# Optimization experiments

Hardware: AMD Instinct MI355X
Metric: run time of the kernel (lower is better)

## Reference

```python
import jax, jax.numpy as jnp
from jax import lax
import numpy as np

# init_kwargs (FlowNet-C canonical config)
K = 1      # kernel_size
MD = 20    # max_displacement
S1 = 1     # stride_1 (input stride)
S2 = 2     # stride_2 (displacement stride)
PAD = 20   # spatial zero padding


def setup_inputs() -> dict:
    key = jax.random.key(0)
    k1, k2 = jax.random.split(key)
    shape = (16, 48, 64, 256)  # [B, H, W, C], channels_last
    return {
        "input_a": jax.random.normal(k1, shape, dtype=jnp.float32),
        "input_b": jax.random.normal(k2, shape, dtype=jnp.float32),
    }


def _corr(a, b):
    # FlowNet correlation cost volume (TFA addons_correlation_cost semantics).
    B, H, W, C = a.shape
    rad = MD // S2                      # displacement radius in stride_2 steps
    D = 2 * rad + 1                     # displacements per axis
    rk = (K - 1) // 2                   # kernel radius
    bd = MD + rk                        # border
    oH = H + 2 * (PAD - bd) // S1       # matches layer's compute_output_shape
    oW = W + 2 * (PAD - bd) // S1
    rows = (oH - 1) * S1 + K            # extent of input needed (pre-pool)
    cols = (oW - 1) * S1 + K

    pa = jnp.pad(a, ((0, 0), (PAD, PAD), (PAD, PAD), (0, 0)))
    pb = jnp.pad(b, ((0, 0), (PAD, PAD), (PAD, PAD), (0, 0)))
    # static region of A covering all kernel windows (centers at h*S1+bd)
    a_reg = lax.slice(pa, (0, bd - rk, bd - rk, 0),
                      (B, bd - rk + rows, bd - rk + cols, C))

    def body(_, d):
        # top_channel d -> (tj, ti) row-major, tj vertical as in TFA kernel
        dy = (d // D) * S2 - MD
        dx = (d % D) * S2 - MD
        b_reg = lax.dynamic_slice(pb, (0, bd - rk + dy, bd - rk + dx, 0),
                                  (B, rows, cols, C))
        p = jnp.sum(a_reg * b_reg, axis=-1)           # [B, rows, cols]
        o = lax.reduce_window(p, 0.0, lax.add,
                              (1, K, K), (1, S1, S1), 'VALID')  # [B, oH, oW]
        return None, o

    # remat keeps scan residuals small (slices recomputed in any backward pass)
    _, outs = lax.scan(jax.checkpoint(body), None, jnp.arange(D * D))
    # [D*D, B, oH, oW] -> [B, oH, oW, D*D]; TFA kernel divides by K*K*C
    return jnp.transpose(outs, (1, 2, 3, 0)) / (K * K * C)


def reference(input_a, input_b):
    return _corr(input_a, input_b)
```

## Files before the change

### kernel.cpp

```cpp
#include <hip/hip_runtime.h>
#include <hip/hip_bf16.h>

#define HH    48
#define WW    64
#define CC    256
#define ND    21
#define OUTD  441
#define PITCH 264
#define SROWS 32

typedef __bf16 v8bf16 __attribute__((ext_vector_type(8)));
typedef float  v4f    __attribute__((ext_vector_type(4)));

__global__ __launch_bounds__(384)
void corr_mfma_kernel(const float* __restrict__ A, const float* __restrict__ B,
                      float* __restrict__ out) {
    __shared__ __bf16 Blds[2][SROWS * PITCH];

    const int blk  = blockIdx.x;
    const int b    = blk >> 5;
    const int rem  = blk & 31;
    const int p    = rem & 1;
    const int hpar = (rem >> 1) & 1;
    const int trip = rem >> 2;
    const int h0   = 6 * trip + hpar;

    const int tid  = threadIdx.x;
    const int lane = tid & 63;
    const int wave = tid >> 6;
    const int mt   = wave & 1;
    const int hr   = wave >> 1;
    const int n    = lane & 15;
    const int quad = lane >> 4;

    const int h = h0 + 2 * hr;

    const int i_lo = (h0 >= 21) ? 0 : ((21 - h0) >> 1);
    const int i_hi = min(22, (67 - h0) >> 1);

    for (int r = 0; r < 3; ++r) {
        int hrow  = h0 + 2 * r;
        int tv_lo = max(0, i_lo - r);
        int tv_hi = min(20, i_hi - r);
        float* outr = out + (size_t)(b * HH + hrow) * WW * OUTD;
        for (int tj = 0; tj < ND; ++tj) {
            if (tj >= tv_lo && tj <= tv_hi) continue;
            for (int idx = tid; idx < 32 * ND; idx += 384) {
                int wp = idx / ND, ti = idx - wp * ND;
                int w  = (wp << 1) + p;
                outr[(size_t)w * OUTD + tj * ND + ti] = 0.f;
            }
        }
    }

    v8bf16 afrag[8];
    {
        int w_a = ((mt * 16 + n) << 1) + p;
        const float* arow = A + ((size_t)(b * HH + h) * WW + w_a) * CC;
        #pragma unroll
        for (int kc = 0; kc < 8; ++kc) {
            int c0 = kc * 32 + quad * 8;
            float4 f0 = *(const float4*)(arow + c0);
            float4 f1 = *(const float4*)(arow + c0 + 4);
            v8bf16 af;
            af[0] = (__bf16)f0.x; af[1] = (__bf16)f0.y; af[2] = (__bf16)f0.z; af[3] = (__bf16)f0.w;
            af[4] = (__bf16)f1.x; af[5] = (__bf16)f1.y; af[6] = (__bf16)f1.z; af[7] = (__bf16)f1.w;
            afrag[kc] = af;
        }
    }

    const float* bimg = B + (size_t)(b * HH) * WW * CC + p * CC;
    float4 pf[6];
    auto load_pf = [&](int hb) {
        const float* brow = bimg + (size_t)hb * WW * CC;
        #pragma unroll
        for (int it = 0; it < 6; ++it) {
            int idx = it * 384 + tid;
            if (idx < 2048)
                pf[it] = *(const float4*)(brow + (idx >> 6) * 2 * CC + ((idx & 63) << 2));
        }
    };
    auto store_lds = [&](int buf) {
        #pragma unroll
        for (int it = 0; it < 6; ++it) {
            int idx = it * 384 + tid;
            if (idx < 2048) {
                __bf16* dst = &Blds[buf][(idx >> 6) * PITCH + ((idx & 63) << 2)];
                dst[0] = (__bf16)pf[it].x; dst[1] = (__bf16)pf[it].y;
                dst[2] = (__bf16)pf[it].z; dst[3] = (__bf16)pf[it].w;
            }
        }
    };

    load_pf(h0 - 20 + 2 * i_lo);
    store_lds(0);
    int cur = 0;

    float* outr = out + (size_t)(b * HH + h) * WW * OUTD;

    for (int i = i_lo; i <= i_hi; ++i) {
        if (i < i_hi) load_pf(h0 - 20 + 2 * (i + 1));
        __syncthreads();

        const int tj = i - hr;
        if ((unsigned)tj <= 20u) {
            const __bf16* bbase = &Blds[cur][n * PITCH + quad * 8];
            v4f acc0 = {0.f, 0.f, 0.f, 0.f};
            v4f acc1 = acc0;
            #pragma unroll
            for (int kc = 0; kc < 8; ++kc) {
                v8bf16 bf0 = *(const v8bf16*)(bbase + kc * 32);
                v8bf16 bf1 = *(const v8bf16*)(bbase + 16 * PITCH + kc * 32);
                acc0 = __builtin_amdgcn_mfma_f32_16x16x32_bf16(afrag[kc], bf0, acc0, 0, 0, 0);
                acc1 = __builtin_amdgcn_mfma_f32_16x16x32_bf16(afrag[kc], bf1, acc1, 0, 0, 0);
            }
            #pragma unroll
            for (int r = 0; r < 4; ++r) {
                int wp = mt * 16 + quad * 4 + r;
                int w  = (wp << 1) + p;
                float* orow = outr + (size_t)w * OUTD + tj * ND;
                int ti0 = 10 + n - wp;
                if ((unsigned)ti0 < 21u) orow[ti0] = acc0[r] * (1.f / 256.f);
                int ti1 = 26 + n - wp;
                if ((unsigned)ti1 < 21u) orow[ti1] = acc1[r] * (1.f / 256.f);
                if (n < 10 - wp)  orow[n]      = 0.f;
                if (n <= wp - 22) orow[20 - n] = 0.f;
            }
        }

        if (i < i_hi) store_lds(cur ^ 1);
        cur ^= 1;
    }
}

extern "C" void kernel_launch(void* const* d_in, const int* in_sizes, int n_in,
                              void* d_out, int out_size, void* d_ws, size_t ws_size,
                              hipStream_t stream) {
    const float* A = (const float*)d_in[0];
    const float* B = (const float*)d_in[1];
    float* out = (float*)d_out;
    dim3 grid(16 * 32);
    dim3 block(384);
    corr_mfma_kernel<<<grid, block, 0, stream>>>(A, B, out);
}
```

Baseline: 210.3 us.

## Split work per output row and tj-half, stage outputs in LDS for coalesced stores

The kernel is reorganised so that each block handles one output row and one half of the vertical displacements. Blocks are remapped across the grid to spread batches over XCDs. Results for all tj are accumulated in registers and then staged through LDS, so each output row is written as contiguous coalesced stores, zeros included. Previously each wave wrote scattered per-element stores plus a separate zero-fill pass. The trade-off is a single-buffered LDS with two barriers per step, larger register pressure from 11 accumulators, and a serial four-pass epilogue.

```diff
diff --git a/kernel.cpp b/kernel.cpp
--- a/kernel.cpp
+++ b/kernel.cpp
@@ -7,51 +7,40 @@
 #define ND    21
 #define OUTD  441
 #define PITCH 264
-#define SROWS 32
+#define PLANE (32 * PITCH)
+#define TJH   11
 
 typedef __bf16 v8bf16 __attribute__((ext_vector_type(8)));
+typedef __bf16 v4bf16 __attribute__((ext_vector_type(4)));
 typedef float  v4f    __attribute__((ext_vector_type(4)));
 
-__global__ __launch_bounds__(384)
+__global__ __launch_bounds__(512, 2)
 void corr_mfma_kernel(const float* __restrict__ A, const float* __restrict__ B,
                       float* __restrict__ out) {
-    __shared__ __bf16 Blds[2][SROWS * PITCH];
+    __shared__ __bf16 Bst[2 * PLANE];
 
-    const int blk  = blockIdx.x;
-    const int b    = blk >> 5;
-    const int rem  = blk & 31;
-    const int p    = rem & 1;
-    const int hpar = (rem >> 1) & 1;
-    const int trip = rem >> 2;
-    const int h0   = 6 * trip + hpar;
+    const int bid = blockIdx.x;
+    const int wg  = (bid & 7) * 192 + (bid >> 3);
+    const int b   = wg / 96;
+    const int rem = wg - b * 96;
+    const int h   = rem >> 1;
+    const int ck  = rem & 1;
 
     const int tid  = threadIdx.x;
     const int lane = tid & 63;
     const int wave = tid >> 6;
-    const int mt   = wave & 1;
-    const int hr   = wave >> 1;
+    const int p    = wave & 1;
+    const int mt   = (wave >> 1) & 1;
+    const int nc   = wave >> 2;
     const int n    = lane & 15;
     const int quad = lane >> 4;
 
-    const int h = h0 + 2 * hr;
-
-    const int i_lo = (h0 >= 21) ? 0 : ((21 - h0) >> 1);
-    const int i_hi = min(22, (67 - h0) >> 1);
-
-    for (int r = 0; r < 3; ++r) {
-        int hrow  = h0 + 2 * r;
-        int tv_lo = max(0, i_lo - r);
-        int tv_hi = min(20, i_hi - r);
-        float* outr = out + (size_t)(b * HH + hrow) * WW * OUTD;
-        for (int tj = 0; tj < ND; ++tj) {
-            if (tj >= tv_lo && tj <= tv_hi) continue;
-            for (int idx = tid; idx < 32 * ND; idx += 384) {
-                int wp = idx / ND, ti = idx - wp * ND;
-                int w  = (wp << 1) + p;
-                outr[(size_t)w * OUTD + tj * ND + ti] = 0.f;
-            }
-        }
-    }
+    const int tj_lo = (h >= 21) ? 0 : ((21 - h) >> 1);
+    const int tj_hi = min(20, (67 - h) >> 1);
+    const int own0  = ck ? 11 : 0;
+    const int n_own = ck ? 10 : 11;
+    const int c_lo  = max(own0, tj_lo);
+    const int c_hi  = min(own0 + n_own - 1, tj_hi);
 
     v8bf16 afrag[8];
     {
@@ -69,67 +58,80 @@
         }
     }
 
-    const float* bimg = B + (size_t)(b * HH) * WW * CC + p * CC;
-    float4 pf[6];
+    const float* bimg = B + (size_t)(b * HH) * WW * CC;
+    float4 pf[8];
     auto load_pf = [&](int hb) {
         const float* brow = bimg + (size_t)hb * WW * CC;
         #pragma unroll
-        for (int it = 0; it < 6; ++it) {
-            int idx = it * 384 + tid;
-            if (idx < 2048)
-                pf[it] = *(const float4*)(brow + (idx >> 6) * 2 * CC + ((idx & 63) << 2));
-        }
+        for (int it = 0; it < 8; ++it)
+            pf[it] = *(const float4*)(brow + 4 * (it * 512 + tid));
     };
-    auto store_lds = [&](int buf) {
+    auto store_lds = [&]() {
         #pragma unroll
-        for (int it = 0; it < 6; ++it) {
-            int idx = it * 384 + tid;
-            if (idx < 2048) {
-                __bf16* dst = &Blds[buf][(idx >> 6) * PITCH + ((idx & 63) << 2)];
-                dst[0] = (__bf16)pf[it].x; dst[1] = (__bf16)pf[it].y;
-                dst[2] = (__bf16)pf[it].z; dst[3] = (__bf16)pf[it].w;
-            }
+        for (int it = 0; it < 8; ++it) {
+            int m  = it * 512 + tid;
+            int j  = m >> 6;
+            int c4 = m & 63;
+            v4bf16 t;
+            t[0] = (__bf16)pf[it].x; t[1] = (__bf16)pf[it].y;
+            t[2] = (__bf16)pf[it].z; t[3] = (__bf16)pf[it].w;
+            *(v4bf16*)&Bst[(j & 1) * PLANE + (j >> 1) * PITCH + c4 * 4] = t;
         }
     };
 
-    load_pf(h0 - 20 + 2 * i_lo);
-    store_lds(0);
-    int cur = 0;
+    v4f acc[TJH];
+    #pragma unroll
+    for (int s = 0; s < TJH; ++s) acc[s] = (v4f){0.f, 0.f, 0.f, 0.f};
 
-    float* outr = out + (size_t)(b * HH + h) * WW * OUTD;
+    if (c_lo <= c_hi) { load_pf(h + 2 * c_lo - 20); store_lds(); }
 
-    for (int i = i_lo; i <= i_hi; ++i) {
-        if (i < i_hi) load_pf(h0 - 20 + 2 * (i + 1));
-        __syncthreads();
+    const __bf16* bb = Bst + p * PLANE + (nc * 16 + n) * PITCH + quad * 8;
 
-        const int tj = i - hr;
-        if ((unsigned)tj <= 20u) {
-            const __bf16* bbase = &Blds[cur][n * PITCH + quad * 8];
-            v4f acc0 = {0.f, 0.f, 0.f, 0.f};
-            v4f acc1 = acc0;
+    #pragma unroll
+    for (int s = 0; s < TJH; ++s) {
+        const int tj = own0 + s;
+        if (tj >= c_lo && tj <= c_hi) {
+            __syncthreads();
+            if (tj < c_hi) load_pf(h + 2 * (tj + 1) - 20);
             #pragma unroll
             for (int kc = 0; kc < 8; ++kc) {
-                v8bf16 bf0 = *(const v8bf16*)(bbase + kc * 32);
-                v8bf16 bf1 = *(const v8bf16*)(bbase + 16 * PITCH + kc * 32);
-                acc0 = __builtin_amdgcn_mfma_f32_16x16x32_bf16(afrag[kc], bf0, acc0, 0, 0, 0);
-                acc1 = __builtin_amdgcn_mfma_f32_16x16x32_bf16(afrag[kc], bf1, acc1, 0, 0, 0);
+                v8bf16 bf = *(const v8bf16*)(bb + kc * 32);
+                acc[s] = __builtin_amdgcn_mfma_f32_16x16x32_bf16(afrag[kc], bf, acc[s], 0, 0, 0);
             }
+            __syncthreads();
+            if (tj < c_hi) store_lds();
+        }
+    }
+
+    __syncthreads();
+    float* ldsf = (float*)Bst;
+    const int nfl = n_own * ND;
+    for (int g = 0; g < 4; ++g) {
+        for (int idx = tid; idx < 16 * TJH * ND; idx += 512) ldsf[idx] = 0.f;
+        __syncthreads();
+        if (mt == (g >> 1) && (quad >> 1) == (g & 1)) {
             #pragma unroll
-            for (int r = 0; r < 4; ++r) {
-                int wp = mt * 16 + quad * 4 + r;
-                int w  = (wp << 1) + p;
-                float* orow = outr + (size_t)w * OUTD + tj * ND;
-                int ti0 = 10 + n - wp;
-                if ((unsigned)ti0 < 21u) orow[ti0] = acc0[r] * (1.f / 256.f);
-                int ti1 = 26 + n - wp;
-                if ((unsigned)ti1 < 21u) orow[ti1] = acc1[r] * (1.f / 256.f);
-                if (n < 10 - wp)  orow[n]      = 0.f;
-                if (n <= wp - 22) orow[20 - n] = 0.f;
+            for (int s = 0; s < TJH; ++s) {
+                if (s < n_own) {
+                    #pragma unroll
+                    for (int q = 0; q < 4; ++q) {
+                        int wp = mt * 16 + quad * 4 + q;
+                        int ti = nc * 16 + n - wp + 10;
+                        if ((unsigned)ti < 21u) {
+                            int lw = (((quad & 1) * 4 + q) << 1) + p;
+                            ldsf[(lw * TJH + s) * ND + ti] = acc[s][q] * (1.f / 256.f);
+                        }
+                    }
+                }
             }
         }
-
-        if (i < i_hi) store_lds(cur ^ 1);
-        cur ^= 1;
+        __syncthreads();
+        float* obase = out + ((size_t)((b * HH + h) * WW) + g * 16) * OUTD + own0 * ND;
+        for (int idx = tid; idx < 16 * nfl; idx += 512) {
+            int lw = idx / nfl, r = idx - lw * nfl;
+            obase[(size_t)lw * OUTD + r] = ldsf[lw * (TJH * ND) + r];
+        }
+        __syncthreads();
     }
 }
 
@@ -139,7 +141,7 @@
     const float* A = (const float*)d_in[0];
     const float* B = (const float*)d_in[1];
     float* out = (float*)d_out;
-    dim3 grid(16 * 32);
-    dim3 block(384);
+    dim3 grid(16 * HH * 2);
+    dim3 block(512);
     corr_mfma_kernel<<<grid, block, 0, stream>>>(A, B, out);
 }
```

Result: slower. 268.3 us (+27.6%).
